# Performance work log

Hardware: AMD Instinct MI355X
Metric: run time of the kernel (lower is better)

The kernel has to match this reference:

```python
import jax, jax.numpy as jnp
import numpy as np

N_NODES = 100000
N_EDGES = 1600000
D_FEAT = 128


def setup_inputs() -> dict:
    key = jax.random.key(0)
    k1, k2, k3 = jax.random.split(key, 3)
    x = jax.random.normal(k1, (N_NODES, D_FEAT), dtype=jnp.float32)
    src = jax.random.randint(k2, (N_EDGES,), 0, N_NODES, dtype=jnp.int64)
    dst = jax.random.randint(k3, (N_EDGES,), 0, N_NODES, dtype=jnp.int64)
    return {"x": x, "src": src, "dst": dst}


def reference(x, src, dst):
    # x: [N, D] node features; src/dst: [E] edge endpoints (edge u->v is src->dst)
    n = x.shape[0]
    # out-degree of every node (clamped to >= 1), matching graph.out_degrees()
    deg = jax.ops.segment_sum(jnp.ones(src.shape[0], dtype=x.dtype), src,
                              num_segments=n)
    deg = jnp.maximum(deg, jnp.asarray(1.0, dtype=x.dtype))
    # per-edge norm: 1/sqrt(deg_out(u) * deg_out(v))  (u_mul_v of out-degrees)
    norm = jax.lax.rsqrt(deg[src] * deg[dst])  # [E]
    # gather-multiply-scatter-sum: out[v] = sum_{(u->v)} x[u] * norm(u,v)
    msg = x[src] * norm[:, None]  # [E, D]
    return jax.ops.segment_sum(msg, dst, num_segments=n)
```

## Files before the change

kernel.cpp:

```cpp
#include <hip/hip_runtime.h>
#include <hip/hip_fp16.h>


#define D_FEAT 128
#define CAP 32
#define NODES_PER_BLOCK 8
#define SS_NODES 50000
#define SS_INTS  12500
#define SC_NODES 25000
#define SC_INTS   6250
#define PCLAMP   200
#define CVTB     512

typedef float f32x4 __attribute__((ext_vector_type(4)));


__global__ void hist_kernel(const int* __restrict__ src, const int* __restrict__ dst,
                            unsigned* __restrict__ H, int E, int N,
                            int nss, int chunkSz, int nc, int histBlocks,
                            const f32x4* __restrict__ x4,
                            ushort4* __restrict__ x16, int n4) {
    int bid = blockIdx.x;
    if (bid >= histBlocks) {
        for (int i = (bid - histBlocks) * (int)blockDim.x + (int)threadIdx.x;
             i < n4; i += CVTB * (int)blockDim.x) {
            f32x4 v = __builtin_nontemporal_load(&x4[i]);
            ushort4 h;
            h.x = __half_as_ushort(__float2half_rn(v.x));
            h.y = __half_as_ushort(__float2half_rn(v.y));
            h.z = __half_as_ushort(__float2half_rn(v.z));
            h.w = __half_as_ushort(__float2half_rn(v.w));
            x16[i] = h;
        }
        return;
    }

    int ax = bid & 1;
    int ss = (bid >> 1) % nss;
    int c  = bid / (2 * nss);
    const int* __restrict__ arr = ax ? dst : src;

    __shared__ unsigned hp[SS_INTS];
    int lo = ss * SS_NODES;
    int span = min(N - lo, SS_NODES);
    for (int i = threadIdx.x; i < SS_INTS; i += blockDim.x) hp[i] = 0u;
    __syncthreads();

    int beg = c * chunkSz;
    int end = min(E, beg + chunkSz);
    int i = beg + (int)threadIdx.x * 4;
    for (; i + 3 < end; i += blockDim.x * 4) {
        int4 v = *reinterpret_cast<const int4*>(&arr[i]);
        unsigned o;
        o = (unsigned)(v.x - lo); if (o < (unsigned)span) atomicAdd(&hp[o >> 2], 1u << (8 * (o & 3)));
        o = (unsigned)(v.y - lo); if (o < (unsigned)span) atomicAdd(&hp[o >> 2], 1u << (8 * (o & 3)));
        o = (unsigned)(v.z - lo); if (o < (unsigned)span) atomicAdd(&hp[o >> 2], 1u << (8 * (o & 3)));
        o = (unsigned)(v.w - lo); if (o < (unsigned)span) atomicAdd(&hp[o >> 2], 1u << (8 * (o & 3)));
    }
    if (i < end) {
        for (int k = i; k < end; ++k) {
            unsigned o = (unsigned)(arr[k] - lo);
            if (o < (unsigned)span) atomicAdd(&hp[o >> 2], 1u << (8 * (o & 3)));
        }
    }
    __syncthreads();

    size_t base = ((size_t)(ax * nss + ss) * nc + c) * SS_INTS;
    for (int j = threadIdx.x; j < SS_INTS; j += blockDim.x) H[base + j] = hp[j];
}

__global__ void scan_kernel(unsigned* __restrict__ H, float* __restrict__ isd,
                            int* __restrict__ cnt, int* __restrict__ novf,
                            int N, int nss, int nc) {
    int total = nss * SS_INTS;
    int g = blockIdx.x * blockDim.x + threadIdx.x;
    if (g == 0) *novf = 0;
    if (g >= 2 * total) return;
    int ax = (g >= total) ? 1 : 0;
    int gg = g - ax * total;
    int ss = gg / SS_INTS;
    int i  = gg - ss * SS_INTS;
    int node0 = ss * SS_NODES + 4 * i;

    size_t base = ((size_t)(ax * nss + ss) * nc) * SS_INTS + i;

    if (ax == 0) {
        int s0 = 0, s1 = 0, s2 = 0, s3 = 0;
        for (int c = 0; c < nc; c += 8) {
            unsigned w[8];
            #pragma unroll
            for (int u = 0; u < 8; ++u) w[u] = H[base + (size_t)(c + u) * SS_INTS];
            #pragma unroll
            for (int u = 0; u < 8; ++u) {
                s0 += w[u] & 255; s1 += (w[u] >> 8) & 255;
                s2 += (w[u] >> 16) & 255; s3 += w[u] >> 24;
            }
        }
        if (node0 + 0 < N) isd[node0 + 0] = rsqrtf(fmaxf((float)s0, 1.0f));
        if (node0 + 1 < N) isd[node0 + 1] = rsqrtf(fmaxf((float)s1, 1.0f));
        if (node0 + 2 < N) isd[node0 + 2] = rsqrtf(fmaxf((float)s2, 1.0f));
        if (node0 + 3 < N) isd[node0 + 3] = rsqrtf(fmaxf((float)s3, 1.0f));
    } else {
        int r0 = 0, r1 = 0, r2 = 0, r3 = 0;
        for (int c = 0; c < nc; c += 8) {
            unsigned w[8];
            #pragma unroll
            for (int u = 0; u < 8; ++u) w[u] = H[base + (size_t)(c + u) * SS_INTS];
            #pragma unroll
            for (int u = 0; u < 8; ++u) {
                unsigned p = (unsigned)min(r0, PCLAMP) | ((unsigned)min(r1, PCLAMP) << 8) |
                             ((unsigned)min(r2, PCLAMP) << 16) | ((unsigned)min(r3, PCLAMP) << 24);
                H[base + (size_t)(c + u) * SS_INTS] = p;
                r0 += w[u] & 255; r1 += (w[u] >> 8) & 255;
                r2 += (w[u] >> 16) & 255; r3 += w[u] >> 24;
            }
        }
        if (node0 + 0 < N) cnt[node0 + 0] = r0;
        if (node0 + 1 < N) cnt[node0 + 1] = r1;
        if (node0 + 2 < N) cnt[node0 + 2] = r2;
        if (node0 + 3 < N) cnt[node0 + 3] = r3;
    }
}

__global__ void scatter_kernel(const int* __restrict__ src, const int* __restrict__ dst,
                               const unsigned* __restrict__ H,
                               int* __restrict__ bucket, int2* __restrict__ ovf,
                               int* __restrict__ novf, int E, int N,
                               int nss, int nsc, int chunkSz, int nc) {
    int bid = blockIdx.x;
    int s = bid % nsc;
    int c = bid / nsc;

    __shared__ unsigned lcp[SC_INTS];
    int lo = s * SC_NODES;
    int span = min(N - lo, SC_NODES);
    int ss = s >> 1;
    size_t base = ((size_t)(nss + ss) * nc + c) * SS_INTS + (size_t)(s & 1) * SC_INTS;
    for (int i = threadIdx.x; i < SC_INTS; i += blockDim.x) lcp[i] = H[base + i];
    __syncthreads();

    int beg = c * chunkSz;
    int end = min(E, beg + chunkSz);
    int i = beg + (int)threadIdx.x * 4;
    for (; i + 3 < end; i += blockDim.x * 4) {
        int4 dv = *reinterpret_cast<const int4*>(&dst[i]);
        int4 sv = *reinterpret_cast<const int4*>(&src[i]);
        #pragma unroll
        for (int k = 0; k < 4; ++k) {
            int d  = (&dv.x)[k];
            int sx = (&sv.x)[k];
            unsigned o = (unsigned)(d - lo);
            if (o < (unsigned)span) {
                int sh = 8 * (o & 3);
                unsigned old = atomicAdd(&lcp[o >> 2], 1u << sh);
                int slot = (old >> sh) & 255;
                if (slot < CAP) {
                    bucket[d * CAP + slot] = sx;
                } else {
                    int ov = atomicAdd(novf, 1);
                    ovf[ov] = make_int2(sx, d);
                }
            }
        }
    }
    if (i < end) {
        for (int k = i; k < end; ++k) {
            int d  = dst[k];
            int sx = src[k];
            unsigned o = (unsigned)(d - lo);
            if (o < (unsigned)span) {
                int sh = 8 * (o & 3);
                unsigned old = atomicAdd(&lcp[o >> 2], 1u << sh);
                int slot = (old >> sh) & 255;
                if (slot < CAP) {
                    bucket[d * CAP + slot] = sx;
                } else {
                    int ov = atomicAdd(novf, 1);
                    ovf[ov] = make_int2(sx, d);
                }
            }
        }
    }
}

__global__ void cvt_kernel(const f32x4* __restrict__ x4,
                           ushort4* __restrict__ x16, int n4) {
    int i = blockIdx.x * blockDim.x + threadIdx.x;
    if (i < n4) {
        f32x4 v = __builtin_nontemporal_load(&x4[i]);
        ushort4 h;
        h.x = __half_as_ushort(__float2half_rn(v.x));
        h.y = __half_as_ushort(__float2half_rn(v.y));
        h.z = __half_as_ushort(__float2half_rn(v.z));
        h.w = __half_as_ushort(__float2half_rn(v.w));
        x16[i] = h;
    }
}

__global__ void gather_kernel(const ushort4* __restrict__ x16,
                              const int* __restrict__ cnt,
                              const int* __restrict__ bucket,
                              const float* __restrict__ isd,
                              f32x4* __restrict__ out4, int N) {
    __shared__ int   sh_idx[NODES_PER_BLOCK * CAP];
    __shared__ float sh_w[NODES_PER_BLOCK * CAP];
    int t = threadIdx.x;
    int node_slot = t >> 5;
    int lane = t & 31;
    int d = blockIdx.x * NODES_PER_BLOCK + node_slot;

    int c = 0;
    if (d < N) {
        c = min(cnt[d], CAP);
        if (lane < c) {
            int s = __builtin_nontemporal_load(&bucket[d * CAP + lane]);
            sh_idx[node_slot * CAP + lane] = s;
            sh_w[node_slot * CAP + lane] = isd[s];
        }
    }
    __syncthreads();
    if (d >= N) return;

    f32x4 acc = {0.f, 0.f, 0.f, 0.f};
    #pragma unroll 8
    for (int k = 0; k < c; ++k) {
        int s   = sh_idx[node_slot * CAP + k];
        float w = sh_w[node_slot * CAP + k];
        ushort4 v = x16[s * 32 + lane];
        acc.x += __half2float(__ushort_as_half(v.x)) * w;
        acc.y += __half2float(__ushort_as_half(v.y)) * w;
        acc.z += __half2float(__ushort_as_half(v.z)) * w;
        acc.w += __half2float(__ushort_as_half(v.w)) * w;
    }
    float wd = isd[d];
    acc.x *= wd; acc.y *= wd; acc.z *= wd; acc.w *= wd;
    __builtin_nontemporal_store(acc, &out4[d * 32 + lane]);
}

__global__ void overflow_kernel(const float* __restrict__ x,
                                const float* __restrict__ isd,
                                const int2* __restrict__ ovf,
                                const int* __restrict__ novf,
                                float* __restrict__ out) {
    int n = *novf;
    for (int e = blockIdx.x; e < n; e += gridDim.x) {
        int2 sd = ovf[e];
        float coef = isd[sd.x] * isd[sd.y];
        atomicAdd(&out[sd.y * D_FEAT + threadIdx.x],
                  x[sd.x * D_FEAT + threadIdx.x] * coef);
    }
}

__global__ void gather32_kernel(const float4* __restrict__ x4,
                                const int* __restrict__ cnt,
                                const int* __restrict__ bucket,
                                const float* __restrict__ isd,
                                float4* __restrict__ out4, int N) {
    __shared__ int   sh_idx[NODES_PER_BLOCK * CAP];
    __shared__ float sh_w[NODES_PER_BLOCK * CAP];
    int t = threadIdx.x;
    int node_slot = t >> 5;
    int lane = t & 31;
    int d = blockIdx.x * NODES_PER_BLOCK + node_slot;

    int c = 0;
    if (d < N) {
        c = min(cnt[d], CAP);
        if (lane < c) {
            int s = bucket[d * CAP + lane];
            sh_idx[node_slot * CAP + lane] = s;
            sh_w[node_slot * CAP + lane] = isd[s];
        }
    }
    __syncthreads();
    if (d >= N) return;

    float4 acc = {0.f, 0.f, 0.f, 0.f};
    #pragma unroll 4
    for (int k = 0; k < c; ++k) {
        int s   = sh_idx[node_slot * CAP + k];
        float w = sh_w[node_slot * CAP + k];
        float4 v = x4[s * 32 + lane];
        acc.x += v.x * w; acc.y += v.y * w;
        acc.z += v.z * w; acc.w += v.w * w;
    }
    float wd = isd[d];
    acc.x *= wd; acc.y *= wd; acc.z *= wd; acc.w *= wd;
    out4[d * 32 + lane] = acc;
}

#define NSLICES_T2 8
#define BPS 512

__global__ void build_kernel(const int* __restrict__ src, const int* __restrict__ dst,
                             int* __restrict__ deg, int* __restrict__ cnt,
                             int* __restrict__ bucket, int2* __restrict__ ovf,
                             int* __restrict__ novf, int E, int sliceSz) {
    int slice = blockIdx.x & (NSLICES_T2 - 1);
    int chunk = blockIdx.x >> 3;
    int lo = slice * sliceSz;
    int hi = lo + sliceSz;
    int chunkSz = (E + BPS - 1) / BPS;
    int beg = chunk * chunkSz;
    int end = min(E, beg + chunkSz);

    for (int i = beg + (int)threadIdx.x; i < end; i += blockDim.x) {
        int s = src[i];
        int d = dst[i];
        if (d >= lo && d < hi) {
            int slot = atomicAdd(&cnt[d], 1);
            if (slot < CAP) {
                bucket[d * CAP + slot] = s;
            } else {
                int o = atomicAdd(novf, 1);
                ovf[o] = make_int2(s, d);
            }
        }
        if (s >= lo && s < hi) {
            atomicAdd(&deg[s], 1);
        }
    }
}

__global__ void isd_kernel(const int* __restrict__ deg, float* __restrict__ isd, int N) {
    int i = blockIdx.x * blockDim.x + threadIdx.x;
    if (i < N) isd[i] = rsqrtf(fmaxf((float)deg[i], 1.0f));
}

__global__ void fb_degree_kernel(const int* __restrict__ src,
                                 float* __restrict__ deg, int E) {
    int i = blockIdx.x * blockDim.x + threadIdx.x;
    if (i < E) atomicAdd(&deg[src[i]], 1.0f);
}
__global__ void fb_inv_sqrt_kernel(float* __restrict__ deg, int N) {
    int i = blockIdx.x * blockDim.x + threadIdx.x;
    if (i < N) deg[i] = rsqrtf(fmaxf(deg[i], 1.0f));
}
__global__ void fb_scatter_kernel(const float* __restrict__ x,
                                  const int* __restrict__ src,
                                  const int* __restrict__ dst,
                                  const float* __restrict__ isd,
                                  float* __restrict__ out, int E) {
    int e = blockIdx.x;
    if (e >= E) return;
    int f = threadIdx.x;
    int s = src[e], d = dst[e];
    float coef = isd[s] * isd[d];
    atomicAdd(&out[(long)d * D_FEAT + f], x[(long)s * D_FEAT + f] * coef);
}

extern "C" void kernel_launch(void* const* d_in, const int* in_sizes, int n_in,
                              void* d_out, int out_size, void* d_ws, size_t ws_size,
                              hipStream_t stream) {
    const float* x   = (const float*)d_in[0];
    const int*   src = (const int*)d_in[1];
    const int*   dst = (const int*)d_in[2];
    float* out = (float*)d_out;

    int N = in_sizes[0] / D_FEAT;
    int E = in_sizes[1];

    int nss = (N + SS_NODES - 1) / SS_NODES;
    int nsc = (N + SC_NODES - 1) / SC_NODES;

    size_t x16Sz = (size_t)N * D_FEAT * 2;
    int n4 = N * (D_FEAT / 4);

    int nc = 0, modeA = 0;
    size_t off_cnt = 0, off_isd = 0, off_misc = 0, off_bucket = 0,
           off_H = 0, off_x16 = 0, off_ovf = 0;
    for (int tryNc = 128; tryNc >= 16 && nc == 0; tryNc >>= 1) {
        size_t hSz = (size_t)2 * nss * tryNc * SS_INTS * 4;
        size_t cA  = 0;
        off_cnt    = cA;                         cA += (size_t)N * 4;
        off_isd    = cA;                         cA += (size_t)N * 4;
        off_misc   = cA;                         cA += 64;
        off_bucket = cA;                         cA += (size_t)N * CAP * 4;
        off_H      = cA;
        size_t a_x16 = off_H + hSz;
        size_t a_ovf = a_x16 + x16Sz;
        size_t a_need = a_ovf + (size_t)E * 8;
        if (ws_size >= a_need) {
            nc = tryNc; modeA = 1; off_x16 = a_x16; off_ovf = a_ovf;
            break;
        }
        size_t uSz = hSz > x16Sz ? hSz : x16Sz;
        size_t b_ovf = off_H + uSz;
        size_t b_need = b_ovf + (size_t)E * 8;
        if (ws_size >= b_need) {
            nc = tryNc; modeA = 0; off_x16 = off_H; off_ovf = b_ovf;
            break;
        }
    }

    if (nc > 0) {
        char* ws = (char*)d_ws;
        int*      cnt    = (int*)(ws + off_cnt);
        float*    isd    = (float*)(ws + off_isd);
        int*      novf   = (int*)(ws + off_misc);
        int*      bucket = (int*)(ws + off_bucket);
        unsigned* H      = (unsigned*)(ws + off_H);
        ushort4*  x16    = (ushort4*)(ws + off_x16);
        int2*     ovf    = (int2*)(ws + off_ovf);

        int chunkSz = (((E + nc - 1) / nc) + 3) & ~3;
        int histBlocks = 2 * nss * nc;

        if (modeA) {
            hist_kernel<<<histBlocks + CVTB, 256, 0, stream>>>(
                src, dst, H, E, N, nss, chunkSz, nc, histBlocks,
                (const f32x4*)x, x16, n4);
        } else {
            hist_kernel<<<histBlocks, 256, 0, stream>>>(
                src, dst, H, E, N, nss, chunkSz, nc, histBlocks,
                (const f32x4*)x, x16, 0);
        }
        scan_kernel<<<(2 * nss * SS_INTS + 255) / 256, 256, 0, stream>>>(
            H, isd, cnt, novf, N, nss, nc);
        scatter_kernel<<<nsc * nc, 256, 0, stream>>>(
            src, dst, H, bucket, ovf, novf, E, N, nss, nsc, chunkSz, nc);
        if (!modeA) {
            cvt_kernel<<<(n4 + 255) / 256, 256, 0, stream>>>(
                (const f32x4*)x, x16, n4);
        }
        gather_kernel<<<(N + NODES_PER_BLOCK - 1) / NODES_PER_BLOCK, 256, 0, stream>>>(
            x16, cnt, bucket, isd, (f32x4*)out, N);
        overflow_kernel<<<64, D_FEAT, 0, stream>>>(x, isd, ovf, novf, out);
        return;
    }

    size_t t2_deg    = 0;
    size_t t2_cnt    = t2_deg + (size_t)N * 4;
    size_t t2_isd    = t2_cnt + (size_t)N * 4;
    size_t t2_novf   = t2_isd + (size_t)N * 4;
    size_t t2_bucket = t2_novf + 16;
    size_t t2_ovf    = t2_bucket + (size_t)N * CAP * 4;
    size_t t2_needed = t2_ovf + (size_t)E * 8;

    if (ws_size >= t2_needed) {
        char* ws = (char*)d_ws;
        int*   deg    = (int*)(ws + t2_deg);
        int*   cnt    = (int*)(ws + t2_cnt);
        float* isd    = (float*)(ws + t2_isd);
        int*   novf   = (int*)(ws + t2_novf);
        int*   bucket = (int*)(ws + t2_bucket);
        int2*  ovf    = (int2*)(ws + t2_ovf);

        hipMemsetAsync(ws, 0, t2_novf + 16, stream);
        int sl = (N + NSLICES_T2 - 1) / NSLICES_T2;
        build_kernel<<<NSLICES_T2 * BPS, 256, 0, stream>>>(src, dst, deg, cnt,
                                                           bucket, ovf, novf, E, sl);
        isd_kernel<<<(N + 255) / 256, 256, 0, stream>>>(deg, isd, N);
        gather32_kernel<<<(N + NODES_PER_BLOCK - 1) / NODES_PER_BLOCK, 256, 0, stream>>>(
            (const float4*)x, cnt, bucket, isd, (float4*)out, N);
        overflow_kernel<<<64, D_FEAT, 0, stream>>>(x, isd, ovf, novf, out);
        return;
    }

    float* deg = (float*)d_ws;
    hipMemsetAsync(deg, 0, (size_t)N * sizeof(float), stream);
    hipMemsetAsync(out, 0, (size_t)out_size * sizeof(float), stream);
    fb_degree_kernel<<<(E + 255) / 256, 256, 0, stream>>>(src, deg, E);
    fb_inv_sqrt_kernel<<<(N + 255) / 256, 256, 0, stream>>>(deg, N);
    fb_scatter_kernel<<<E, D_FEAT, 0, stream>>>(x, src, dst, deg, out, E);
}
```

Before: 251.3 us.

## Fuse histogram, scan, scatter and convert into one cooperative kernel with grid syncs

Replaces the separate hist, scan, scatter and fp16-convert launches with one cooperative megakernel whose phases are separated by grid-wide syncs. In modeA the fp16 conversion runs on threads left idle during the scan phase. The aim is to remove several kernel launch gaps and tail bubbles between dependent passes. The cost is that the grid is limited to co-resident blocks (nb = 2*nss*nc), and grid.sync adds barrier overhead. If the cooperative launch fails, the code falls back to the old multi-kernel path.

```diff
diff --git a/kernel.cpp b/kernel.cpp
--- a/kernel.cpp
+++ b/kernel.cpp
@@ -1,6 +1,9 @@
 #include <hip/hip_runtime.h>
 #include <hip/hip_fp16.h>
-
+#include <hip/hip_cooperative_groups.h>
+
+
+namespace cg = cooperative_groups;
 
 #define D_FEAT 128
 #define CAP 32
@@ -14,6 +17,188 @@
 
 typedef float f32x4 __attribute__((ext_vector_type(4)));
 
+__device__ __forceinline__ void cvt_range(const f32x4* __restrict__ x4,
+                                          ushort4* __restrict__ x16,
+                                          int start, int stride, int n4) {
+    for (int i = start; i < n4; i += stride) {
+        f32x4 v = __builtin_nontemporal_load(&x4[i]);
+        ushort4 h;
+        h.x = __half_as_ushort(__float2half_rn(v.x));
+        h.y = __half_as_ushort(__float2half_rn(v.y));
+        h.z = __half_as_ushort(__float2half_rn(v.z));
+        h.w = __half_as_ushort(__float2half_rn(v.w));
+        x16[i] = h;
+    }
+}
+
+__global__ void __launch_bounds__(256, 2)
+build_mega(const int* __restrict__ src, const int* __restrict__ dst,
+           unsigned* __restrict__ H, float* __restrict__ isd,
+           int* __restrict__ cnt, int* __restrict__ novf,
+           int* __restrict__ bucket, int2* __restrict__ ovf,
+           const f32x4* __restrict__ x4, ushort4* __restrict__ x16,
+           int n4, int modeA,
+           int E, int N, int nss, int nsc, int chunkSz, int nc) {
+    cg::grid_group grid = cg::this_grid();
+    __shared__ unsigned lds[SS_INTS];
+    int bid = blockIdx.x;
+    int nb  = gridDim.x;
+    int tid = (int)threadIdx.x;
+
+    {
+        int ax = bid & 1;
+        int ss = (bid >> 1) % nss;
+        int c  = bid / (2 * nss);
+        const int* __restrict__ arr = ax ? dst : src;
+        int lo = ss * SS_NODES;
+        int span = min(N - lo, SS_NODES);
+        for (int i = tid; i < SS_INTS; i += blockDim.x) lds[i] = 0u;
+        __syncthreads();
+
+        int beg = c * chunkSz;
+        int end = min(E, beg + chunkSz);
+        int i = beg + tid * 4;
+        for (; i + 3 < end; i += blockDim.x * 4) {
+            int4 v = *reinterpret_cast<const int4*>(&arr[i]);
+            unsigned o;
+            o = (unsigned)(v.x - lo); if (o < (unsigned)span) atomicAdd(&lds[o >> 2], 1u << (8 * (o & 3)));
+            o = (unsigned)(v.y - lo); if (o < (unsigned)span) atomicAdd(&lds[o >> 2], 1u << (8 * (o & 3)));
+            o = (unsigned)(v.z - lo); if (o < (unsigned)span) atomicAdd(&lds[o >> 2], 1u << (8 * (o & 3)));
+            o = (unsigned)(v.w - lo); if (o < (unsigned)span) atomicAdd(&lds[o >> 2], 1u << (8 * (o & 3)));
+        }
+        if (i < end) {
+            for (int k = i; k < end; ++k) {
+                unsigned o = (unsigned)(arr[k] - lo);
+                if (o < (unsigned)span) atomicAdd(&lds[o >> 2], 1u << (8 * (o & 3)));
+            }
+        }
+        __syncthreads();
+
+        size_t base = ((size_t)(ax * nss + ss) * nc + c) * SS_INTS;
+        for (int j = tid; j < SS_INTS; j += blockDim.x) H[base + j] = lds[j];
+        if (bid == 0 && tid == 0) *novf = 0;
+    }
+    grid.sync();
+
+    {
+        int total = nss * SS_INTS;
+        int S = 2 * total;
+        int T = nb * (int)blockDim.x;
+        int g = bid * (int)blockDim.x + tid;
+        if (g < S) {
+            int ax = (g >= total) ? 1 : 0;
+            int gg = g - ax * total;
+            int ss = gg / SS_INTS;
+            int i  = gg - ss * SS_INTS;
+            int node0 = ss * SS_NODES + 4 * i;
+            size_t base = ((size_t)(ax * nss + ss) * nc) * SS_INTS + i;
+
+            if (ax == 0) {
+                int s0 = 0, s1 = 0, s2 = 0, s3 = 0;
+                for (int c = 0; c < nc; c += 8) {
+                    unsigned w[8];
+                    #pragma unroll
+                    for (int u = 0; u < 8; ++u) w[u] = H[base + (size_t)(c + u) * SS_INTS];
+                    #pragma unroll
+                    for (int u = 0; u < 8; ++u) {
+                        s0 += w[u] & 255; s1 += (w[u] >> 8) & 255;
+                        s2 += (w[u] >> 16) & 255; s3 += w[u] >> 24;
+                    }
+                }
+                if (node0 + 0 < N) isd[node0 + 0] = rsqrtf(fmaxf((float)s0, 1.0f));
+                if (node0 + 1 < N) isd[node0 + 1] = rsqrtf(fmaxf((float)s1, 1.0f));
+                if (node0 + 2 < N) isd[node0 + 2] = rsqrtf(fmaxf((float)s2, 1.0f));
+                if (node0 + 3 < N) isd[node0 + 3] = rsqrtf(fmaxf((float)s3, 1.0f));
+            } else {
+                int r0 = 0, r1 = 0, r2 = 0, r3 = 0;
+                for (int c = 0; c < nc; c += 8) {
+                    unsigned w[8];
+                    #pragma unroll
+                    for (int u = 0; u < 8; ++u) w[u] = H[base + (size_t)(c + u) * SS_INTS];
+                    #pragma unroll
+                    for (int u = 0; u < 8; ++u) {
+                        unsigned p = (unsigned)min(r0, PCLAMP) | ((unsigned)min(r1, PCLAMP) << 8) |
+                                     ((unsigned)min(r2, PCLAMP) << 16) | ((unsigned)min(r3, PCLAMP) << 24);
+                        H[base + (size_t)(c + u) * SS_INTS] = p;
+                        r0 += w[u] & 255; r1 += (w[u] >> 8) & 255;
+                        r2 += (w[u] >> 16) & 255; r3 += w[u] >> 24;
+                    }
+                }
+                if (node0 + 0 < N) cnt[node0 + 0] = r0;
+                if (node0 + 1 < N) cnt[node0 + 1] = r1;
+                if (node0 + 2 < N) cnt[node0 + 2] = r2;
+                if (node0 + 3 < N) cnt[node0 + 3] = r3;
+            }
+        } else if (modeA) {
+            cvt_range(x4, x16, g - S, T - S, n4);
+        }
+    }
+    grid.sync();
+
+    {
+        int s = bid % nsc;
+        int c = bid / nsc;
+        if (c < nc) {
+            int lo = s * SC_NODES;
+            int span = min(N - lo, SC_NODES);
+            int ss = s >> 1;
+            size_t base = ((size_t)(nss + ss) * nc + c) * SS_INTS + (size_t)(s & 1) * SC_INTS;
+            for (int i = tid; i < SC_INTS; i += blockDim.x) lds[i] = H[base + i];
+            __syncthreads();
+
+            int beg = c * chunkSz;
+            int end = min(E, beg + chunkSz);
+            int i = beg + tid * 4;
+            for (; i + 3 < end; i += blockDim.x * 4) {
+                int4 dv = *reinterpret_cast<const int4*>(&dst[i]);
+                int4 sv = *reinterpret_cast<const int4*>(&src[i]);
+                #pragma unroll
+                for (int k = 0; k < 4; ++k) {
+                    int d  = (&dv.x)[k];
+                    int sx = (&sv.x)[k];
+                    unsigned o = (unsigned)(d - lo);
+                    if (o < (unsigned)span) {
+                        int sh = 8 * (o & 3);
+                        unsigned old = atomicAdd(&lds[o >> 2], 1u << sh);
+                        int slot = (old >> sh) & 255;
+                        if (slot < CAP) {
+                            bucket[d * CAP + slot] = sx;
+                        } else {
+                            int ov = atomicAdd(novf, 1);
+                            ovf[ov] = make_int2(sx, d);
+                        }
+                    }
+                }
+            }
+            if (i < end) {
+                for (int k = i; k < end; ++k) {
+                    int d  = dst[k];
+                    int sx = src[k];
+                    unsigned o = (unsigned)(d - lo);
+                    if (o < (unsigned)span) {
+                        int sh = 8 * (o & 3);
+                        unsigned old = atomicAdd(&lds[o >> 2], 1u << sh);
+                        int slot = (old >> sh) & 255;
+                        if (slot < CAP) {
+                            bucket[d * CAP + slot] = sx;
+                        } else {
+                            int ov = atomicAdd(novf, 1);
+                            ovf[ov] = make_int2(sx, d);
+                        }
+                    }
+                }
+            }
+        }
+    }
+
+    if (!modeA) {
+        grid.sync();
+        int T = nb * (int)blockDim.x;
+        int g = bid * (int)blockDim.x + tid;
+        cvt_range(x4, x16, g, T, n4);
+    }
+}
+
 
 __global__ void hist_kernel(const int* __restrict__ src, const int* __restrict__ dst,
                             unsigned* __restrict__ H, int E, int N,
@@ -22,19 +207,10 @@
                             ushort4* __restrict__ x16, int n4) {
     int bid = blockIdx.x;
     if (bid >= histBlocks) {
-        for (int i = (bid - histBlocks) * (int)blockDim.x + (int)threadIdx.x;
-             i < n4; i += CVTB * (int)blockDim.x) {
-            f32x4 v = __builtin_nontemporal_load(&x4[i]);
-            ushort4 h;
-            h.x = __half_as_ushort(__float2half_rn(v.x));
-            h.y = __half_as_ushort(__float2half_rn(v.y));
-            h.z = __half_as_ushort(__float2half_rn(v.z));
-            h.w = __half_as_ushort(__float2half_rn(v.w));
-            x16[i] = h;
-        }
+        cvt_range(x4, x16, (bid - histBlocks) * (int)blockDim.x + (int)threadIdx.x,
+                  CVTB * (int)blockDim.x, n4);
         return;
     }
-
     int ax = bid & 1;
     int ss = (bid >> 1) % nss;
     int c  = bid / (2 * nss);
@@ -81,7 +257,6 @@
     int ss = gg / SS_INTS;
     int i  = gg - ss * SS_INTS;
     int node0 = ss * SS_NODES + 4 * i;
-
     size_t base = ((size_t)(ax * nss + ss) * nc) * SS_INTS + i;
 
     if (ax == 0) {
@@ -186,15 +361,7 @@
 __global__ void cvt_kernel(const f32x4* __restrict__ x4,
                            ushort4* __restrict__ x16, int n4) {
     int i = blockIdx.x * blockDim.x + threadIdx.x;
-    if (i < n4) {
-        f32x4 v = __builtin_nontemporal_load(&x4[i]);
-        ushort4 h;
-        h.x = __half_as_ushort(__float2half_rn(v.x));
-        h.y = __half_as_ushort(__float2half_rn(v.y));
-        h.z = __half_as_ushort(__float2half_rn(v.z));
-        h.w = __half_as_ushort(__float2half_rn(v.w));
-        x16[i] = h;
-    }
+    if (i < n4) cvt_range(x4, x16, i, n4, n4);
 }
 
 __global__ void gather_kernel(const ushort4* __restrict__ x16,
@@ -404,25 +571,41 @@
         int2*     ovf    = (int2*)(ws + off_ovf);
 
         int chunkSz = (((E + nc - 1) / nc) + 3) & ~3;
-        int histBlocks = 2 * nss * nc;
-
-        if (modeA) {
-            hist_kernel<<<histBlocks + CVTB, 256, 0, stream>>>(
-                src, dst, H, E, N, nss, chunkSz, nc, histBlocks,
-                (const f32x4*)x, x16, n4);
-        } else {
-            hist_kernel<<<histBlocks, 256, 0, stream>>>(
-                src, dst, H, E, N, nss, chunkSz, nc, histBlocks,
-                (const f32x4*)x, x16, 0);
-        }
-        scan_kernel<<<(2 * nss * SS_INTS + 255) / 256, 256, 0, stream>>>(
-            H, isd, cnt, novf, N, nss, nc);
-        scatter_kernel<<<nsc * nc, 256, 0, stream>>>(
-            src, dst, H, bucket, ovf, novf, E, N, nss, nsc, chunkSz, nc);
-        if (!modeA) {
-            cvt_kernel<<<(n4 + 255) / 256, 256, 0, stream>>>(
-                (const f32x4*)x, x16, n4);
-        }
+        int nb = 2 * nss * nc;
+
+        const f32x4* x4 = (const f32x4*)x;
+        const int* src_ = src;
+        const int* dst_ = dst;
+        void* args[] = { (void*)&src_, (void*)&dst_, (void*)&H, (void*)&isd,
+                         (void*)&cnt, (void*)&novf, (void*)&bucket, (void*)&ovf,
+                         (void*)&x4, (void*)&x16, (void*)&n4, (void*)&modeA,
+                         (void*)&E, (void*)&N, (void*)&nss, (void*)&nsc,
+                         (void*)&chunkSz, (void*)&nc };
+        hipError_t cerr = hipLaunchCooperativeKernel(
+            reinterpret_cast<void*>(build_mega), dim3(nb), dim3(256),
+            args, 0, stream);
+
+        if (cerr != hipSuccess) {
+            int histBlocks = nb;
+            if (modeA) {
+                hist_kernel<<<histBlocks + CVTB, 256, 0, stream>>>(
+                    src, dst, H, E, N, nss, chunkSz, nc, histBlocks,
+                    (const f32x4*)x, x16, n4);
+            } else {
+                hist_kernel<<<histBlocks, 256, 0, stream>>>(
+                    src, dst, H, E, N, nss, chunkSz, nc, histBlocks,
+                    (const f32x4*)x, x16, 0);
+            }
+            scan_kernel<<<(2 * nss * SS_INTS + 255) / 256, 256, 0, stream>>>(
+                H, isd, cnt, novf, N, nss, nc);
+            scatter_kernel<<<nsc * nc, 256, 0, stream>>>(
+                src, dst, H, bucket, ovf, novf, E, N, nss, nsc, chunkSz, nc);
+            if (!modeA) {
+                cvt_kernel<<<(n4 + 255) / 256, 256, 0, stream>>>(
+                    (const f32x4*)x, x16, n4);
+            }
+        }
+
         gather_kernel<<<(N + NODES_PER_BLOCK - 1) / NODES_PER_BLOCK, 256, 0, stream>>>(
             x16, cnt, bucket, isd, (f32x4*)out, N);
         overflow_kernel<<<64, D_FEAT, 0, stream>>>(x, isd, ovf, novf, out);
```

After: 401.6 us. +59.8%, slower.
